# Kernel optimization log

Measured on AMD Instinct MI355X. Metric: run time of the kernel, lower is better.

## Reference

```python
import jax, jax.numpy as jnp
import numpy as np

N_NODES = 100000
N_EDGES = 1600000
IN_FEATS = 128
OUT_FEATS = 32


def setup_inputs() -> dict:
    key = jax.random.key(0)
    k1, k2, k3, k4 = jax.random.split(key, 4)
    inputs = jax.random.normal(k1, (N_NODES, IN_FEATS), dtype=jnp.float32)
    weight = jax.random.normal(k2, (IN_FEATS, OUT_FEATS), dtype=jnp.float32)
    src = jax.random.randint(k3, (N_EDGES,), 0, N_NODES, dtype=jnp.int32)
    dst = jax.random.randint(k4, (N_EDGES,), 0, N_NODES, dtype=jnp.int32)
    return {"inputs": inputs, "weight": weight, "src": src, "dst": dst}


def reference(inputs, weight, src, dst):
    # GCNLayer.forward: dense projection then sparse sum-aggregation (gspmmv,
    # no normalization: norm flags False/False -> plain neighbor sum).
    h = inputs @ weight                      # [N, out_feats]
    msgs = h[src]                            # gather over edges [E, out_feats]
    out = jax.ops.segment_sum(msgs, dst, num_segments=inputs.shape[0])
    return out
```

## Files before the change

kernel.cpp:

```cpp
#include <hip/hip_runtime.h>
#include <hip/hip_bf16.h>

#define N_F_IN 128
#define N_F_OUT 32

#define BSHIFT 7
#define BNODES 128
#define BCAP 2560
#define SCAT_EDGES 4096
#define NBL 1024
#define OFFT_LD 400

typedef __attribute__((ext_vector_type(8))) short short8v;
typedef __attribute__((ext_vector_type(4))) float float4v;

static __device__ __forceinline__ unsigned bf16pair(float a, float b) {
    unsigned ua = __float_as_uint(a), ub = __float_as_uint(b);
    ua = (ua + 0x7FFFu + ((ua >> 16) & 1u)) >> 16;
    ub = (ub + 0x7FFFu + ((ub >> 16) & 1u)) >> 16;
    return ua | (ub << 16);
}
static __device__ __forceinline__ unsigned short bf16r(float a) {
    unsigned ua = __float_as_uint(a);
    return (unsigned short)((ua + 0x7FFFu + ((ua >> 16) & 1u)) >> 16);
}

union SharedU {
    unsigned short wT[32 * 136];
    struct {
        int A[NBL];
        int B[NBL];
        int wsum[8];
        int lrec[SCAT_EDGES];
    } sc;
};

__global__ __launch_bounds__(512, 8) void phaseA_kernel(const float* __restrict__ x,
                                                        const float* __restrict__ w,
                                                        unsigned short* __restrict__ hb,
                                                        int n,
                                                        const int* __restrict__ src,
                                                        const int* __restrict__ dst,
                                                        int* __restrict__ recs,
                                                        unsigned short* __restrict__ offT,
                                                        int E, int nsc) {
    __shared__ SharedU u;
    const int t = threadIdx.x;
    const int lane = t & 63;
    const int wvid = t >> 6;

    if ((int)blockIdx.x < nsc) {
        const int chunk = blockIdx.x;
        const int e0 = chunk * SCAT_EDGES;
        const int cnt = min(SCAT_EDGES, E - e0);

        int dv[8], sv[8];
        #pragma unroll
        for (int j = 0; j < 8; ++j) {
            int i = t + j * 512;
            dv[j] = -1; sv[j] = 0;
            if (i < cnt) { dv[j] = dst[e0 + i]; sv[j] = src[e0 + i]; }
        }

        for (int i = t; i < NBL; i += 512) u.sc.A[i] = 0;
        __syncthreads();

        #pragma unroll
        for (int j = 0; j < 8; ++j)
            if (dv[j] >= 0) atomicAdd(&u.sc.A[dv[j] >> BSHIFT], 1);
        __syncthreads();

        const int b0 = t * 2;
        const int c0 = u.sc.A[b0], c1 = u.sc.A[b0 + 1];
        const int tot = c0 + c1;
        int sc = tot;
        #pragma unroll
        for (int off = 1; off < 64; off <<= 1) {
            int v = __shfl_up(sc, off, 64);
            if (lane >= off) sc += v;
        }
        if (lane == 63) u.sc.wsum[wvid] = sc;
        __syncthreads();
        int wbase = 0;
        #pragma unroll
        for (int ww = 0; ww < 7; ++ww) wbase += (ww < wvid) ? u.sc.wsum[ww] : 0;
        const int base = wbase + sc - tot;
        u.sc.B[b0] = base;
        u.sc.B[b0 + 1] = base + c0;
        offT[(long)b0 * OFFT_LD + chunk]       = (unsigned short)base;
        offT[(long)(b0 + 1) * OFFT_LD + chunk] = (unsigned short)(base + c0);
        __syncthreads();

        #pragma unroll
        for (int j = 0; j < 8; ++j) {
            if (dv[j] >= 0) {
                int r = atomicAdd(&u.sc.B[dv[j] >> BSHIFT], 1);
                u.sc.lrec[r] = ((dv[j] & (BNODES - 1)) << 17) | sv[j];
            }
        }
        __syncthreads();

        {
            int* rp = recs + (long)chunk * SCAT_EDGES;
            const int4* lr4 = (const int4*)u.sc.lrec;
            int4* rp4 = (int4*)rp;
            const int c4 = cnt >> 2;
            for (int i = t; i < c4; i += 512) rp4[i] = lr4[i];
            for (int i = (c4 << 2) + t; i < cnt; i += 512) rp[i] = u.sc.lrec[i];
        }
        return;
    }

    {
        const float4* w4 = (const float4*)w;
        const float4 wa = w4[t * 2], wb = w4[t * 2 + 1];
        int idx = t * 8;
        u.wT[((idx + 0) & 31) * 136 + ((idx + 0) >> 5)] = bf16r(wa.x);
        u.wT[((idx + 1) & 31) * 136 + ((idx + 1) >> 5)] = bf16r(wa.y);
        u.wT[((idx + 2) & 31) * 136 + ((idx + 2) >> 5)] = bf16r(wa.z);
        u.wT[((idx + 3) & 31) * 136 + ((idx + 3) >> 5)] = bf16r(wa.w);
        u.wT[((idx + 4) & 31) * 136 + ((idx + 4) >> 5)] = bf16r(wb.x);
        u.wT[((idx + 5) & 31) * 136 + ((idx + 5) >> 5)] = bf16r(wb.y);
        u.wT[((idx + 6) & 31) * 136 + ((idx + 6) >> 5)] = bf16r(wb.z);
        u.wT[((idx + 7) & 31) * 136 + ((idx + 7) >> 5)] = bf16r(wb.w);
    }
    __syncthreads();

    const int lr = lane & 15;
    const int lg = lane >> 4;
    const int ntiles = (n + 15) >> 4;
    const int mtile = ((int)blockIdx.x - nsc) * 8 + wvid;
    if (mtile < ntiles) {
        const long R0 = (long)mtile * 16;
        long rr = R0 + lr; if (rr >= n) rr = n - 1;
        const float4* q = (const float4*)(x + rr * N_F_IN) + lg * 2;

        const unsigned short* wr0 = &u.wT[lr * 136];
        const unsigned short* wr1 = &u.wT[(16 + lr) * 136];

        float4 p0 = q[0], p1 = q[1], p2 = q[8], p3 = q[9];
        float4v acc0 = {0.f, 0.f, 0.f, 0.f}, acc1 = {0.f, 0.f, 0.f, 0.f};
        #pragma unroll
        for (int ks = 0; ks < 4; ++ks) {
            float4 lo, hi;
            if (ks & 1) { lo = p2; hi = p3; } else { lo = p0; hi = p1; }
            union { short8v v; unsigned uu[4]; } af;
            af.uu[0] = bf16pair(lo.x, lo.y);
            af.uu[1] = bf16pair(lo.z, lo.w);
            af.uu[2] = bf16pair(hi.x, hi.y);
            af.uu[3] = bf16pair(hi.z, hi.w);
            if (ks == 0) { p0 = q[16]; p1 = q[17]; }
            if (ks == 1) { p2 = q[24]; p3 = q[25]; }
            short8v bf0 = *(const short8v*)(wr0 + ks * 32 + lg * 8);
            short8v bf1 = *(const short8v*)(wr1 + ks * 32 + lg * 8);
            acc0 = __builtin_amdgcn_mfma_f32_16x16x32_bf16(af.v, bf0, acc0, 0, 0, 0);
            acc1 = __builtin_amdgcn_mfma_f32_16x16x32_bf16(af.v, bf1, acc1, 0, 0, 0);
        }
        #pragma unroll
        for (int reg = 0; reg < 4; ++reg) {
            long row = R0 + lg * 4 + reg;
            if (row < n) {
                hb[row * N_F_OUT + lr]      = bf16r(acc0[reg]);
                hb[row * N_F_OUT + 16 + lr] = bf16r(acc1[reg]);
            }
        }
    }
}

__global__ __launch_bounds__(512) void agg_kernel(const unsigned short* __restrict__ hb,
                                                  const unsigned short* __restrict__ offT,
                                                  const int* __restrict__ recs,
                                                  float* __restrict__ out, int n, int nch) {
    __shared__ unsigned short s_st[OFFT_LD];
    __shared__ int dof[512];
    __shared__ int srt0[BCAP];
    __shared__ int srt[BCAP];
    __shared__ int cN[BNODES], loff[BNODES + 1], lc[BNODES], wsum8[8];
    __shared__ int s_tot;
    const int t = threadIdx.x;
    const int b = blockIdx.x;
    const int lane = t & 63;
    const int wv = t >> 6;

    for (int i = t; i < nch; i += 512) s_st[i] = offT[(long)b * OFFT_LD + i];
    int en_t = (t < nch) ? (int)offT[(long)(b + 1) * OFFT_LD + t] : 0;
    if (t < BNODES) cN[t] = 0;
    __syncthreads();

    const int cc = (t < nch) ? (en_t - (int)s_st[t]) : 0;
    int sc = cc;
    #pragma unroll
    for (int off = 1; off < 64; off <<= 1) {
        int v = __shfl_up(sc, off, 64);
        if (lane >= off) sc += v;
    }
    if (lane == 63) wsum8[wv] = sc;
    __syncthreads();
    int wbase = 0;
    #pragma unroll
    for (int ww = 0; ww < 7; ++ww) wbase += (ww < wv) ? wsum8[ww] : 0;
    dof[t] = wbase + sc - cc;
    if (t == 511) s_tot = wbase + sc;
    __syncthreads();
    const int cnt = min(s_tot, BCAP);

    for (int i = t; i < cnt; i += 512) {
        int lo = 0, hi = nch;
        while (hi - lo > 1) {
            int mid = (lo + hi) >> 1;
            if (dof[mid] <= i) lo = mid; else hi = mid;
        }
        int v = recs[(long)lo * SCAT_EDGES + (int)s_st[lo] + (i - dof[lo])];
        srt0[i] = v;
        atomicAdd(&cN[(v >> 17) & (BNODES - 1)], 1);
    }
    __syncthreads();

    if (t < 64) {
        int v0 = cN[2 * t], v1 = cN[2 * t + 1];
        int s = v0 + v1;
        #pragma unroll
        for (int off = 1; off < 64; off <<= 1) {
            int v = __shfl_up(s, off, 64);
            if (t >= off) s += v;
        }
        int ex = s - v0 - v1;
        loff[2 * t] = ex;
        loff[2 * t + 1] = ex + v0;
        lc[2 * t] = ex;
        lc[2 * t + 1] = ex + v0;
        if (t == 63) loff[BNODES] = s;
    }
    __syncthreads();

    int i = t;
    for (; i + 1536 < cnt; i += 2048) {
        int r0 = srt0[i],        r1 = srt0[i + 512];
        int r2 = srt0[i + 1024], r3 = srt0[i + 1536];
        int k0 = atomicAdd(&lc[(r0 >> 17) & (BNODES - 1)], 1); srt[k0] = r0 & 0x1FFFF;
        int k1 = atomicAdd(&lc[(r1 >> 17) & (BNODES - 1)], 1); srt[k1] = r1 & 0x1FFFF;
        int k2 = atomicAdd(&lc[(r2 >> 17) & (BNODES - 1)], 1); srt[k2] = r2 & 0x1FFFF;
        int k3 = atomicAdd(&lc[(r3 >> 17) & (BNODES - 1)], 1); srt[k3] = r3 & 0x1FFFF;
    }
    for (; i < cnt; i += 512) {
        int r0 = srt0[i];
        int k0 = atomicAdd(&lc[(r0 >> 17) & (BNODES - 1)], 1); srt[k0] = r0 & 0x1FFFF;
    }
    __syncthreads();

    const uint2* hq = (const uint2*)hb;
    #pragma unroll
    for (int pp = 0; pp < 2; ++pp) {
        int nl = pp * 64 + (t >> 3);
        int jj = t & 7;
        int beg = loff[nl], end = loff[nl + 1];
        float4 a0 = make_float4(0.f, 0.f, 0.f, 0.f);
        float4 a1 = a0;
        int k = beg;
        for (; k + 8 <= end; k += 8) {
            uint2 v0 = hq[(size_t)srt[k] * 8 + jj];
            uint2 v1 = hq[(size_t)srt[k + 1] * 8 + jj];
            uint2 v2 = hq[(size_t)srt[k + 2] * 8 + jj];
            uint2 v3 = hq[(size_t)srt[k + 3] * 8 + jj];
            uint2 v4 = hq[(size_t)srt[k + 4] * 8 + jj];
            uint2 v5 = hq[(size_t)srt[k + 5] * 8 + jj];
            uint2 v6 = hq[(size_t)srt[k + 6] * 8 + jj];
            uint2 v7 = hq[(size_t)srt[k + 7] * 8 + jj];
            a0.x += __uint_as_float(v0.x << 16); a0.y += __uint_as_float(v0.x & 0xFFFF0000u);
            a0.z += __uint_as_float(v0.y << 16); a0.w += __uint_as_float(v0.y & 0xFFFF0000u);
            a1.x += __uint_as_float(v1.x << 16); a1.y += __uint_as_float(v1.x & 0xFFFF0000u);
            a1.z += __uint_as_float(v1.y << 16); a1.w += __uint_as_float(v1.y & 0xFFFF0000u);
            a0.x += __uint_as_float(v2.x << 16); a0.y += __uint_as_float(v2.x & 0xFFFF0000u);
            a0.z += __uint_as_float(v2.y << 16); a0.w += __uint_as_float(v2.y & 0xFFFF0000u);
            a1.x += __uint_as_float(v3.x << 16); a1.y += __uint_as_float(v3.x & 0xFFFF0000u);
            a1.z += __uint_as_float(v3.y << 16); a1.w += __uint_as_float(v3.y & 0xFFFF0000u);
            a0.x += __uint_as_float(v4.x << 16); a0.y += __uint_as_float(v4.x & 0xFFFF0000u);
            a0.z += __uint_as_float(v4.y << 16); a0.w += __uint_as_float(v4.y & 0xFFFF0000u);
            a1.x += __uint_as_float(v5.x << 16); a1.y += __uint_as_float(v5.x & 0xFFFF0000u);
            a1.z += __uint_as_float(v5.y << 16); a1.w += __uint_as_float(v5.y & 0xFFFF0000u);
            a0.x += __uint_as_float(v6.x << 16); a0.y += __uint_as_float(v6.x & 0xFFFF0000u);
            a0.z += __uint_as_float(v6.y << 16); a0.w += __uint_as_float(v6.y & 0xFFFF0000u);
            a1.x += __uint_as_float(v7.x << 16); a1.y += __uint_as_float(v7.x & 0xFFFF0000u);
            a1.z += __uint_as_float(v7.y << 16); a1.w += __uint_as_float(v7.y & 0xFFFF0000u);
        }
        for (; k + 4 <= end; k += 4) {
            uint2 v0 = hq[(size_t)srt[k] * 8 + jj];
            uint2 v1 = hq[(size_t)srt[k + 1] * 8 + jj];
            uint2 v2 = hq[(size_t)srt[k + 2] * 8 + jj];
            uint2 v3 = hq[(size_t)srt[k + 3] * 8 + jj];
            a0.x += __uint_as_float(v0.x << 16); a0.y += __uint_as_float(v0.x & 0xFFFF0000u);
            a0.z += __uint_as_float(v0.y << 16); a0.w += __uint_as_float(v0.y & 0xFFFF0000u);
            a1.x += __uint_as_float(v1.x << 16); a1.y += __uint_as_float(v1.x & 0xFFFF0000u);
            a1.z += __uint_as_float(v1.y << 16); a1.w += __uint_as_float(v1.y & 0xFFFF0000u);
            a0.x += __uint_as_float(v2.x << 16); a0.y += __uint_as_float(v2.x & 0xFFFF0000u);
            a0.z += __uint_as_float(v2.y << 16); a0.w += __uint_as_float(v2.y & 0xFFFF0000u);
            a1.x += __uint_as_float(v3.x << 16); a1.y += __uint_as_float(v3.x & 0xFFFF0000u);
            a1.z += __uint_as_float(v3.y << 16); a1.w += __uint_as_float(v3.y & 0xFFFF0000u);
        }
        for (; k < end; ++k) {
            uint2 v0 = hq[(size_t)srt[k] * 8 + jj];
            a0.x += __uint_as_float(v0.x << 16); a0.y += __uint_as_float(v0.x & 0xFFFF0000u);
            a0.z += __uint_as_float(v0.y << 16); a0.w += __uint_as_float(v0.y & 0xFFFF0000u);
        }
        float4 a = make_float4(a0.x + a1.x, a0.y + a1.y, a0.z + a1.z, a0.w + a1.w);
        long node = (long)b * BNODES + nl;
        if (node < n) *(float4*)&out[node * N_F_OUT + jj * 4] = a;
    }
}

extern "C" void kernel_launch(void* const* d_in, const int* in_sizes, int n_in,
                              void* d_out, int out_size, void* d_ws, size_t ws_size,
                              hipStream_t stream) {
    const float* x = (const float*)d_in[0];
    const float* w = (const float*)d_in[1];
    const int* src = (const int*)d_in[2];
    const int* dst = (const int*)d_in[3];
    float* out = (float*)d_out;

    const int n = in_sizes[0] / N_F_IN;
    const int E = in_sizes[2];
    const int NB = (n + BNODES - 1) >> BSHIFT;
    const int nch = (E + SCAT_EDGES - 1) / SCAT_EDGES;

    char* p = (char*)d_ws;
    unsigned short* hb = (unsigned short*)p;
    p += (((size_t)n * N_F_OUT * sizeof(unsigned short)) + 255) & ~(size_t)255;
    int* recs = (int*)p;
    p += (((size_t)nch * SCAT_EDGES * sizeof(int)) + 255) & ~(size_t)255;
    unsigned short* offT = (unsigned short*)p;
    p += (((size_t)1025 * OFFT_LD * sizeof(unsigned short)) + 255) & ~(size_t)255;

    const int ntiles = (n + 15) >> 4;
    const int ngemm = (ntiles + 7) >> 3;
    const int nblk = nch + ngemm;

    phaseA_kernel<<<nblk, 512, 0, stream>>>(x, w, hb, n, src, dst, recs, offT, E, nch);
    agg_kernel<<<NB, 512, 0, stream>>>(hb, offT, recs, out, n, nch);
}
```

Before: 52.35 us.

## Split pipeline into three kernels, overlapping half the GEMM with bucket sorting

Result: slower. 56.88 us (+8.6%).

```diff
diff --git a/kernel.cpp b/kernel.cpp
--- a/kernel.cpp
+++ b/kernel.cpp
@@ -10,6 +10,7 @@
 #define SCAT_EDGES 4096
 #define NBL 1024
 #define OFFT_LD 400
+#define LOFF_LD 132
 
 typedef __attribute__((ext_vector_type(8))) short short8v;
 typedef __attribute__((ext_vector_type(4))) float float4v;
@@ -25,7 +26,62 @@
     return (unsigned short)((ua + 0x7FFFu + ((ua >> 16) & 1u)) >> 16);
 }
 
-union SharedU {
+static __device__ __forceinline__ void stage_w(unsigned short* wT, const float* __restrict__ w, int t) {
+    const float4* w4 = (const float4*)w;
+    const float4 wa = w4[t * 2], wb = w4[t * 2 + 1];
+    int idx = t * 8;
+    wT[((idx + 0) & 31) * 136 + ((idx + 0) >> 5)] = bf16r(wa.x);
+    wT[((idx + 1) & 31) * 136 + ((idx + 1) >> 5)] = bf16r(wa.y);
+    wT[((idx + 2) & 31) * 136 + ((idx + 2) >> 5)] = bf16r(wa.z);
+    wT[((idx + 3) & 31) * 136 + ((idx + 3) >> 5)] = bf16r(wa.w);
+    wT[((idx + 4) & 31) * 136 + ((idx + 4) >> 5)] = bf16r(wb.x);
+    wT[((idx + 5) & 31) * 136 + ((idx + 5) >> 5)] = bf16r(wb.y);
+    wT[((idx + 6) & 31) * 136 + ((idx + 6) >> 5)] = bf16r(wb.z);
+    wT[((idx + 7) & 31) * 136 + ((idx + 7) >> 5)] = bf16r(wb.w);
+}
+
+static __device__ __forceinline__ void gemm_tile(const float* __restrict__ x,
+                                                 unsigned short* __restrict__ hb,
+                                                 int n, const unsigned short* wT,
+                                                 int mtile, int lr, int lg) {
+    const int ntiles = (n + 15) >> 4;
+    if (mtile >= ntiles) return;
+    const long R0 = (long)mtile * 16;
+    long rr = R0 + lr; if (rr >= n) rr = n - 1;
+    const float4* q = (const float4*)(x + rr * N_F_IN) + lg * 2;
+
+    const unsigned short* wr0 = &wT[lr * 136];
+    const unsigned short* wr1 = &wT[(16 + lr) * 136];
+
+    float4 p0 = q[0], p1 = q[1], p2 = q[8], p3 = q[9];
+    float4v acc0 = {0.f, 0.f, 0.f, 0.f}, acc1 = {0.f, 0.f, 0.f, 0.f};
+    #pragma unroll
+    for (int ks = 0; ks < 4; ++ks) {
+        float4 lo, hi;
+        if (ks & 1) { lo = p2; hi = p3; } else { lo = p0; hi = p1; }
+        union { short8v v; unsigned uu[4]; } af;
+        af.uu[0] = bf16pair(lo.x, lo.y);
+        af.uu[1] = bf16pair(lo.z, lo.w);
+        af.uu[2] = bf16pair(hi.x, hi.y);
+        af.uu[3] = bf16pair(hi.z, hi.w);
+        if (ks == 0) { p0 = q[16]; p1 = q[17]; }
+        if (ks == 1) { p2 = q[24]; p3 = q[25]; }
+        short8v bf0 = *(const short8v*)(wr0 + ks * 32 + lg * 8);
+        short8v bf1 = *(const short8v*)(wr1 + ks * 32 + lg * 8);
+        acc0 = __builtin_amdgcn_mfma_f32_16x16x32_bf16(af.v, bf0, acc0, 0, 0, 0);
+        acc1 = __builtin_amdgcn_mfma_f32_16x16x32_bf16(af.v, bf1, acc1, 0, 0, 0);
+    }
+    #pragma unroll
+    for (int reg = 0; reg < 4; ++reg) {
+        long row = R0 + lg * 4 + reg;
+        if (row < n) {
+            hb[row * N_F_OUT + lr]      = bf16r(acc0[reg]);
+            hb[row * N_F_OUT + 16 + lr] = bf16r(acc1[reg]);
+        }
+    }
+}
+
+union SharedA {
     unsigned short wT[32 * 136];
     struct {
         int A[NBL];
@@ -35,7 +91,7 @@
     } sc;
 };
 
-__global__ __launch_bounds__(512, 8) void phaseA_kernel(const float* __restrict__ x,
+__global__ __launch_bounds__(512, 8) void phase1_kernel(const float* __restrict__ x,
                                                         const float* __restrict__ w,
                                                         unsigned short* __restrict__ hb,
                                                         int n,
@@ -44,7 +100,7 @@
                                                         int* __restrict__ recs,
                                                         unsigned short* __restrict__ offT,
                                                         int E, int nsc) {
-    __shared__ SharedU u;
+    __shared__ SharedA u;
     const int t = threadIdx.x;
     const int lane = t & 63;
     const int wvid = t >> 6;
@@ -111,113 +167,82 @@
         return;
     }
 
-    {
-        const float4* w4 = (const float4*)w;
-        const float4 wa = w4[t * 2], wb = w4[t * 2 + 1];
-        int idx = t * 8;
-        u.wT[((idx + 0) & 31) * 136 + ((idx + 0) >> 5)] = bf16r(wa.x);
-        u.wT[((idx + 1) & 31) * 136 + ((idx + 1) >> 5)] = bf16r(wa.y);
-        u.wT[((idx + 2) & 31) * 136 + ((idx + 2) >> 5)] = bf16r(wa.z);
-        u.wT[((idx + 3) & 31) * 136 + ((idx + 3) >> 5)] = bf16r(wa.w);
-        u.wT[((idx + 4) & 31) * 136 + ((idx + 4) >> 5)] = bf16r(wb.x);
-        u.wT[((idx + 5) & 31) * 136 + ((idx + 5) >> 5)] = bf16r(wb.y);
-        u.wT[((idx + 6) & 31) * 136 + ((idx + 6) >> 5)] = bf16r(wb.z);
-        u.wT[((idx + 7) & 31) * 136 + ((idx + 7) >> 5)] = bf16r(wb.w);
-    }
-    __syncthreads();
-
-    const int lr = lane & 15;
-    const int lg = lane >> 4;
-    const int ntiles = (n + 15) >> 4;
-    const int mtile = ((int)blockIdx.x - nsc) * 8 + wvid;
-    if (mtile < ntiles) {
-        const long R0 = (long)mtile * 16;
-        long rr = R0 + lr; if (rr >= n) rr = n - 1;
-        const float4* q = (const float4*)(x + rr * N_F_IN) + lg * 2;
-
-        const unsigned short* wr0 = &u.wT[lr * 136];
-        const unsigned short* wr1 = &u.wT[(16 + lr) * 136];
-
-        float4 p0 = q[0], p1 = q[1], p2 = q[8], p3 = q[9];
-        float4v acc0 = {0.f, 0.f, 0.f, 0.f}, acc1 = {0.f, 0.f, 0.f, 0.f};
-        #pragma unroll
-        for (int ks = 0; ks < 4; ++ks) {
-            float4 lo, hi;
-            if (ks & 1) { lo = p2; hi = p3; } else { lo = p0; hi = p1; }
-            union { short8v v; unsigned uu[4]; } af;
-            af.uu[0] = bf16pair(lo.x, lo.y);
-            af.uu[1] = bf16pair(lo.z, lo.w);
-            af.uu[2] = bf16pair(hi.x, hi.y);
-            af.uu[3] = bf16pair(hi.z, hi.w);
-            if (ks == 0) { p0 = q[16]; p1 = q[17]; }
-            if (ks == 1) { p2 = q[24]; p3 = q[25]; }
-            short8v bf0 = *(const short8v*)(wr0 + ks * 32 + lg * 8);
-            short8v bf1 = *(const short8v*)(wr1 + ks * 32 + lg * 8);
-            acc0 = __builtin_amdgcn_mfma_f32_16x16x32_bf16(af.v, bf0, acc0, 0, 0, 0);
-            acc1 = __builtin_amdgcn_mfma_f32_16x16x32_bf16(af.v, bf1, acc1, 0, 0, 0);
-        }
-        #pragma unroll
-        for (int reg = 0; reg < 4; ++reg) {
-            long row = R0 + lg * 4 + reg;
-            if (row < n) {
-                hb[row * N_F_OUT + lr]      = bf16r(acc0[reg]);
-                hb[row * N_F_OUT + 16 + lr] = bf16r(acc1[reg]);
-            }
-        }
-    }
-}
-
-__global__ __launch_bounds__(512) void agg_kernel(const unsigned short* __restrict__ hb,
-                                                  const unsigned short* __restrict__ offT,
-                                                  const int* __restrict__ recs,
-                                                  float* __restrict__ out, int n, int nch) {
-    __shared__ unsigned short s_st[OFFT_LD];
-    __shared__ int dof[512];
-    __shared__ int srt0[BCAP];
-    __shared__ int srt[BCAP];
-    __shared__ int cN[BNODES], loff[BNODES + 1], lc[BNODES], wsum8[8];
-    __shared__ int s_tot;
+    stage_w(u.wT, w, t);
+    __syncthreads();
+    gemm_tile(x, hb, n, u.wT, ((int)blockIdx.x - nsc) * 8 + wvid, lane & 15, lane >> 4);
+}
+
+union SharedB {
+    unsigned short wT[32 * 136];
+    struct {
+        unsigned short st[OFFT_LD];
+        int dof[512];
+        int srt0[BCAP];
+        int srt[BCAP];
+        int cN[BNODES], loff[BNODES + 1], lc[BNODES], wsum8[8];
+        int tot;
+    } ag;
+};
+
+__global__ __launch_bounds__(512, 8) void phase2_kernel(const float* __restrict__ x,
+                                                        const float* __restrict__ w,
+                                                        unsigned short* __restrict__ hb,
+                                                        int n,
+                                                        const unsigned short* __restrict__ offT,
+                                                        const int* __restrict__ recs,
+                                                        int* __restrict__ srtg,
+                                                        int* __restrict__ loffg,
+                                                        int nch, int ng2, int tile0) {
+    __shared__ SharedB u;
     const int t = threadIdx.x;
-    const int b = blockIdx.x;
     const int lane = t & 63;
     const int wv = t >> 6;
 
-    for (int i = t; i < nch; i += 512) s_st[i] = offT[(long)b * OFFT_LD + i];
+    if ((int)blockIdx.x < ng2) {
+        stage_w(u.wT, w, t);
+        __syncthreads();
+        gemm_tile(x, hb, n, u.wT, tile0 + (int)blockIdx.x * 8 + wv, lane & 15, lane >> 4);
+        return;
+    }
+
+    const int b = (int)blockIdx.x - ng2;
+
+    for (int i = t; i < nch; i += 512) u.ag.st[i] = offT[(long)b * OFFT_LD + i];
     int en_t = (t < nch) ? (int)offT[(long)(b + 1) * OFFT_LD + t] : 0;
-    if (t < BNODES) cN[t] = 0;
-    __syncthreads();
-
-    const int cc = (t < nch) ? (en_t - (int)s_st[t]) : 0;
+    if (t < BNODES) u.ag.cN[t] = 0;
+    __syncthreads();
+
+    const int cc = (t < nch) ? (en_t - (int)u.ag.st[t]) : 0;
     int sc = cc;
     #pragma unroll
     for (int off = 1; off < 64; off <<= 1) {
         int v = __shfl_up(sc, off, 64);
         if (lane >= off) sc += v;
     }
-    if (lane == 63) wsum8[wv] = sc;
+    if (lane == 63) u.ag.wsum8[wv] = sc;
     __syncthreads();
     int wbase = 0;
     #pragma unroll
-    for (int ww = 0; ww < 7; ++ww) wbase += (ww < wv) ? wsum8[ww] : 0;
-    dof[t] = wbase + sc - cc;
-    if (t == 511) s_tot = wbase + sc;
-    __syncthreads();
-    const int cnt = min(s_tot, BCAP);
+    for (int ww = 0; ww < 7; ++ww) wbase += (ww < wv) ? u.ag.wsum8[ww] : 0;
+    u.ag.dof[t] = wbase + sc - cc;
+    if (t == 511) u.ag.tot = wbase + sc;
+    __syncthreads();
+    const int cnt = min(u.ag.tot, BCAP);
 
     for (int i = t; i < cnt; i += 512) {
         int lo = 0, hi = nch;
         while (hi - lo > 1) {
             int mid = (lo + hi) >> 1;
-            if (dof[mid] <= i) lo = mid; else hi = mid;
-        }
-        int v = recs[(long)lo * SCAT_EDGES + (int)s_st[lo] + (i - dof[lo])];
-        srt0[i] = v;
-        atomicAdd(&cN[(v >> 17) & (BNODES - 1)], 1);
+            if (u.ag.dof[mid] <= i) lo = mid; else hi = mid;
+        }
+        int v = recs[(long)lo * SCAT_EDGES + (int)u.ag.st[lo] + (i - u.ag.dof[lo])];
+        u.ag.srt0[i] = v;
+        atomicAdd(&u.ag.cN[(v >> 17) & (BNODES - 1)], 1);
     }
     __syncthreads();
 
     if (t < 64) {
-        int v0 = cN[2 * t], v1 = cN[2 * t + 1];
+        int v0 = u.ag.cN[2 * t], v1 = u.ag.cN[2 * t + 1];
         int s = v0 + v1;
         #pragma unroll
         for (int off = 1; off < 64; off <<= 1) {
@@ -225,26 +250,54 @@
             if (t >= off) s += v;
         }
         int ex = s - v0 - v1;
-        loff[2 * t] = ex;
-        loff[2 * t + 1] = ex + v0;
-        lc[2 * t] = ex;
-        lc[2 * t + 1] = ex + v0;
-        if (t == 63) loff[BNODES] = s;
+        u.ag.loff[2 * t] = ex;
+        u.ag.loff[2 * t + 1] = ex + v0;
+        u.ag.lc[2 * t] = ex;
+        u.ag.lc[2 * t + 1] = ex + v0;
+        if (t == 63) u.ag.loff[BNODES] = s;
     }
     __syncthreads();
 
     int i = t;
     for (; i + 1536 < cnt; i += 2048) {
-        int r0 = srt0[i],        r1 = srt0[i + 512];
-        int r2 = srt0[i + 1024], r3 = srt0[i + 1536];
-        int k0 = atomicAdd(&lc[(r0 >> 17) & (BNODES - 1)], 1); srt[k0] = r0 & 0x1FFFF;
-        int k1 = atomicAdd(&lc[(r1 >> 17) & (BNODES - 1)], 1); srt[k1] = r1 & 0x1FFFF;
-        int k2 = atomicAdd(&lc[(r2 >> 17) & (BNODES - 1)], 1); srt[k2] = r2 & 0x1FFFF;
-        int k3 = atomicAdd(&lc[(r3 >> 17) & (BNODES - 1)], 1); srt[k3] = r3 & 0x1FFFF;
+        int r0 = u.ag.srt0[i],        r1 = u.ag.srt0[i + 512];
+        int r2 = u.ag.srt0[i + 1024], r3 = u.ag.srt0[i + 1536];
+        int k0 = atomicAdd(&u.ag.lc[(r0 >> 17) & (BNODES - 1)], 1); u.ag.srt[k0] = r0 & 0x1FFFF;
+        int k1 = atomicAdd(&u.ag.lc[(r1 >> 17) & (BNODES - 1)], 1); u.ag.srt[k1] = r1 & 0x1FFFF;
+        int k2 = atomicAdd(&u.ag.lc[(r2 >> 17) & (BNODES - 1)], 1); u.ag.srt[k2] = r2 & 0x1FFFF;
+        int k3 = atomicAdd(&u.ag.lc[(r3 >> 17) & (BNODES - 1)], 1); u.ag.srt[k3] = r3 & 0x1FFFF;
     }
     for (; i < cnt; i += 512) {
-        int r0 = srt0[i];
-        int k0 = atomicAdd(&lc[(r0 >> 17) & (BNODES - 1)], 1); srt[k0] = r0 & 0x1FFFF;
+        int r0 = u.ag.srt0[i];
+        int k0 = atomicAdd(&u.ag.lc[(r0 >> 17) & (BNODES - 1)], 1); u.ag.srt[k0] = r0 & 0x1FFFF;
+    }
+    __syncthreads();
+
+    {
+        int4* sg = (int4*)(srtg + (size_t)b * BCAP);
+        const int4* ls = (const int4*)u.ag.srt;
+        const int c4 = (cnt + 3) >> 2;
+        for (int k = t; k < c4; k += 512) sg[k] = ls[k];
+        if (t <= BNODES) loffg[b * LOFF_LD + t] = u.ag.loff[t];
+    }
+}
+
+__global__ __launch_bounds__(512) void pull_kernel(const unsigned short* __restrict__ hb,
+                                                   const int* __restrict__ srtg,
+                                                   const int* __restrict__ loffg,
+                                                   float* __restrict__ out, int n) {
+    __shared__ int srt[BCAP];
+    __shared__ int loff[BNODES + 1];
+    const int t = threadIdx.x;
+    const int b = blockIdx.x;
+
+    const int cnt = loffg[b * LOFF_LD + BNODES];
+    {
+        const int4* sg = (const int4*)(srtg + (size_t)b * BCAP);
+        int4* ls = (int4*)srt;
+        const int c4 = (cnt + 3) >> 2;
+        for (int k = t; k < c4; k += 512) ls[k] = sg[k];
+        if (t <= BNODES) loff[t] = loffg[b * LOFF_LD + t];
     }
     __syncthreads();
 
@@ -329,11 +382,19 @@
     p += (((size_t)nch * SCAT_EDGES * sizeof(int)) + 255) & ~(size_t)255;
     unsigned short* offT = (unsigned short*)p;
     p += (((size_t)1025 * OFFT_LD * sizeof(unsigned short)) + 255) & ~(size_t)255;
+    int* srtg = (int*)p;
+    p += (((size_t)NB * BCAP * sizeof(int)) + 255) & ~(size_t)255;
+    int* loffg = (int*)p;
+    p += (((size_t)NB * LOFF_LD * sizeof(int)) + 255) & ~(size_t)255;
 
     const int ntiles = (n + 15) >> 4;
-    const int ngemm = (ntiles + 7) >> 3;
-    const int nblk = nch + ngemm;
-
-    phaseA_kernel<<<nblk, 512, 0, stream>>>(x, w, hb, n, src, dst, recs, offT, E, nch);
-    agg_kernel<<<NB, 512, 0, stream>>>(hb, offT, recs, out, n, nch);
-}
+    const int ng = (ntiles + 7) >> 3;
+    const int ng1 = ng >> 1;
+    const int ng2 = ng - ng1;
+    const int tile0 = ng1 * 8;
+
+    phase1_kernel<<<nch + ng1, 512, 0, stream>>>(x, w, hb, n, src, dst, recs, offT, E, nch);
+    phase2_kernel<<<ng2 + NB, 512, 0, stream>>>(x, w, hb, n, offT, recs, srtg, loffg,
+                                                nch, ng2, tile0);
+    pull_kernel<<<NB, 512, 0, stream>>>(hb, srtg, loffg, out, n);
+}
```
